# Kernel tuning notes

Measured on AMD Instinct MI355X. Metric: run time of the kernel, lower is better.

The kernel has to match this reference:

```python
import jax, jax.numpy as jnp
import numpy as np

B, C, N = 4, 64, 512
H = 128  # hidden width; MLP input is 2*C = 128


def setup_inputs() -> dict:
    key = jax.random.key(0)
    k0, k1, k2 = jax.random.split(key, 3)
    x = jax.random.normal(k0, (B, C, N), dtype=jnp.float32)
    # Torch Linear init ~ U(-1/sqrt(fan_in), 1/sqrt(fan_in)); stored as (in, out) for einsum.
    W1 = jax.random.normal(k1, (2 * C, H), dtype=jnp.float32) * (1.0 / np.sqrt(2 * C))
    b1 = jnp.zeros((H,), dtype=jnp.float32)
    W2 = jax.random.normal(k2, (H, 1), dtype=jnp.float32) * (1.0 / np.sqrt(H))
    b2 = jnp.zeros((1,), dtype=jnp.float32)
    return {"x": x, "W1": W1, "b1": b1, "W2": W2, "b2": b2}


def reference(x, W1, b1, W2, b2):
    # x: (B, C, N). Equivalent to the per-offset loop: for every pair (i, j) with
    # j > i, score = MLP(concat(x[:, :, i], x[:, :, j])), placed at y[:, i, j].
    # Dropout is identity in eval mode.
    b, c, n = x.shape
    xt = jnp.transpose(x, (0, 2, 1))                      # (B, N, C)
    left = jnp.broadcast_to(xt[:, :, None, :], (b, n, n, c))   # row index i
    right = jnp.broadcast_to(xt[:, None, :, :], (b, n, n, c))  # col index j
    pairs = jnp.concatenate([left, right], axis=-1)       # (B, N, N, 2C)
    h = jax.nn.relu(jnp.einsum('bijc,ch->bijh', pairs, W1) + b1)
    score = (jnp.einsum('bijh,ho->bijo', h, W2) + b2)[..., 0]  # (B, N, N)
    mask = jnp.triu(jnp.ones((n, n), dtype=score.dtype), k=1)  # strict upper triangle
    return score * mask
```

## Files before the change

### kernel.cpp

```cpp
#include <hip/hip_runtime.h>

#define B_ 4
#define C_ 64
#define N_ 512
#define H_ 128

typedef float v2f __attribute__((ext_vector_type(2)));
typedef float v4f __attribute__((ext_vector_type(4)));

__global__ __launch_bounds__(256) void proj_kernel(
    const float* __restrict__ x, const float* __restrict__ W1,
    const float* __restrict__ b1, float* __restrict__ Lbuf,
    float* __restrict__ Rbuf)
{
    __shared__ float Wl[64 * 128];
    __shared__ float xs[16 * 68];

    const int t    = threadIdx.x;
    const int half = blockIdx.x >> 7;
    const int rem  = blockIdx.x & 127;
    const int b    = rem >> 5;
    const int i0   = (rem & 31) * 16;
    const int cbase = half * 64;

    const float4* W14 = (const float4*)W1;
    float4* Wl4 = (float4*)Wl;
    #pragma unroll
    for (int k = 0; k < 8; ++k)
        Wl4[t + k * 256] = W14[cbase * 32 + t + k * 256];

    #pragma unroll
    for (int k = 0; k < 4; ++k) {
        int idx = t + k * 256;
        int c = idx >> 4, ii = idx & 15;
        xs[ii * 68 + c] = x[b * (C_ * N_) + c * N_ + i0 + ii];
    }
    __syncthreads();

    const int hq  = t & 31;
    const int il  = (t >> 5) * 2;
    const int col = hq * 4;

    v2f a0l = {0.f, 0.f}, a0h = {0.f, 0.f};
    if (half) {
        float4 bv = *(const float4*)(b1 + col);
        a0l = {bv.x, bv.y};
        a0h = {bv.z, bv.w};
    }
    v2f a1l = a0l, a1h = a0h;

    const v4f* Wlv = (const v4f*)Wl;
    #pragma unroll
    for (int c = 0; c < 64; c += 4) {
        float4 xv0 = *(float4*)(xs + il * 68 + c);
        float4 xv1 = *(float4*)(xs + (il + 1) * 68 + c);
        const float* x0p = (const float*)&xv0;
        const float* x1p = (const float*)&xv1;
        #pragma unroll
        for (int cc = 0; cc < 4; ++cc) {
            v4f wv = Wlv[(c + cc) * 32 + hq];
            v2f wl = wv.xy, wh = wv.zw;
            v2f xb0 = {x0p[cc], x0p[cc]};
            v2f xb1 = {x1p[cc], x1p[cc]};
            a0l = __builtin_elementwise_fma(wl, xb0, a0l);
            a0h = __builtin_elementwise_fma(wh, xb0, a0h);
            a1l = __builtin_elementwise_fma(wl, xb1, a1l);
            a1h = __builtin_elementwise_fma(wh, xb1, a1h);
        }
    }

    float* buf = half ? Rbuf : Lbuf;
    float* o = buf + b * (N_ * H_) + (i0 + il) * H_ + col;
    *(float4*)o        = make_float4(a0l.x, a0l.y, a0h.x, a0h.y);
    *(float4*)(o + H_) = make_float4(a1l.x, a1l.y, a1h.x, a1h.y);
}

__global__ __launch_bounds__(256) void pair_kernel(
    const float* __restrict__ Lbuf, const float* __restrict__ Rbuf,
    const float* __restrict__ W2, const float* __restrict__ b2,
    float* __restrict__ out)
{
    __shared__ v4f Lt4[32 * 32];
    __shared__ v4f Rt4[32 * 32];

    const int t = threadIdx.x;
    int b, it, jt;
    {
        int bid = blockIdx.x;
        if (bid >= 544) {
            int z = bid - 544;
            b = z & 3;
            int k = z >> 2;
            it = 1;
            while (k >= it) { k -= it; ++it; }
            jt = k;
            float* outb = out + b * (N_ * N_);
            const int r = t >> 3, cq = t & 7;
            *(float4*)(outb + (it * 32 + r) * N_ + jt * 32 + cq * 4) =
                make_float4(0.f, 0.f, 0.f, 0.f);
            return;
        }
        b = bid & 3;
        int k = bid >> 2;
        it = 0;
        while (k >= 16 - it) { k -= 16 - it; ++it; }
        jt = it + k;
    }
    const int ti0 = it * 32, tj0 = jt * 32;
    float* outb = out + b * (N_ * N_);

    const float* Lsrc = Lbuf + b * (N_ * H_) + ti0 * H_;
    const float* Rsrc = Rbuf + b * (N_ * H_) + tj0 * H_;
    #pragma unroll
    for (int kk = 0; kk < 4; ++kk) {
        int idx = t + kk * 256;
        int row = idx >> 5, hc = idx & 31;
        int sc = hc ^ (row >> 2);
        Lt4[row * 32 + sc] = *(const v4f*)(Lsrc + row * H_ + hc * 4);
        Rt4[row * 32 + sc] = *(const v4f*)(Rsrc + row * H_ + hc * 4);
    }
    __syncthreads();

    const int w    = t >> 6;
    const int lane = t & 63;
    const int til  = (w >> 1) * 16 + (lane >> 3) * 2;
    const int tjl  = (w & 1) * 16 + (lane & 7) * 2;
    const int rotL = til >> 2;
    const int rotR = tjl >> 2;

    const v4f* Lp  = Lt4 + til * 32;
    const v4f* Rp  = Rt4 + tjl * 32;
    const v4f* W24 = (const v4f*)W2;

    v2f c00l = {0.f, 0.f}, c00h = {0.f, 0.f};
    v2f c01l = {0.f, 0.f}, c01h = {0.f, 0.f};
    v2f c10l = {0.f, 0.f}, c10h = {0.f, 0.f};
    v2f c11l = {0.f, 0.f}, c11h = {0.f, 0.f};

    #pragma unroll 8
    for (int hc = 0; hc < 32; ++hc) {
        const int oL = hc ^ rotL;
        const int oR = hc ^ rotR;
        v4f L0 = Lp[oL];
        v4f L1 = Lp[32 + oL];
        v4f R0 = Rp[oR];
        v4f R1 = Rp[32 + oR];
        v4f wv = W24[hc];
        v2f wl = wv.xy, wh = wv.zw;
        const v2f z2 = {0.f, 0.f};
        v2f s;
        s = __builtin_elementwise_max(L0.xy + R0.xy, z2);
        c00l = __builtin_elementwise_fma(s, wl, c00l);
        s = __builtin_elementwise_max(L0.zw + R0.zw, z2);
        c00h = __builtin_elementwise_fma(s, wh, c00h);
        s = __builtin_elementwise_max(L0.xy + R1.xy, z2);
        c01l = __builtin_elementwise_fma(s, wl, c01l);
        s = __builtin_elementwise_max(L0.zw + R1.zw, z2);
        c01h = __builtin_elementwise_fma(s, wh, c01h);
        s = __builtin_elementwise_max(L1.xy + R0.xy, z2);
        c10l = __builtin_elementwise_fma(s, wl, c10l);
        s = __builtin_elementwise_max(L1.zw + R0.zw, z2);
        c10h = __builtin_elementwise_fma(s, wh, c10h);
        s = __builtin_elementwise_max(L1.xy + R1.xy, z2);
        c11l = __builtin_elementwise_fma(s, wl, c11l);
        s = __builtin_elementwise_max(L1.zw + R1.zw, z2);
        c11h = __builtin_elementwise_fma(s, wh, c11h);
    }

    const float bias2 = b2[0];
    float a00 = (c00l.x + c00l.y) + (c00h.x + c00h.y);
    float a01 = (c01l.x + c01l.y) + (c01h.x + c01h.y);
    float a10 = (c10l.x + c10l.y) + (c10h.x + c10h.y);
    float a11 = (c11l.x + c11l.y) + (c11h.x + c11h.y);

    const int gi0 = ti0 + til, gj0 = tj0 + tjl;
    float2 v0, v1;
    v0.x = (gj0     > gi0    ) ? (a00 + bias2) : 0.f;
    v0.y = (gj0 + 1 > gi0    ) ? (a01 + bias2) : 0.f;
    v1.x = (gj0     > gi0 + 1) ? (a10 + bias2) : 0.f;
    v1.y = (gj0 + 1 > gi0 + 1) ? (a11 + bias2) : 0.f;
    *(float2*)(outb + gi0 * N_ + gj0) = v0;
    *(float2*)(outb + (gi0 + 1) * N_ + gj0) = v1;
}

extern "C" void kernel_launch(void* const* d_in, const int* in_sizes, int n_in,
                              void* d_out, int out_size, void* d_ws, size_t ws_size,
                              hipStream_t stream)
{
    const float* x  = (const float*)d_in[0];
    const float* W1 = (const float*)d_in[1];
    const float* b1 = (const float*)d_in[2];
    const float* W2 = (const float*)d_in[3];
    const float* b2 = (const float*)d_in[4];
    float* out  = (float*)d_out;
    float* Lbuf = (float*)d_ws;
    float* Rbuf = Lbuf + B_ * N_ * H_;

    proj_kernel<<<256, 256, 0, stream>>>(x, W1, b1, Lbuf, Rbuf);
    pair_kernel<<<B_ * 256, 256, 0, stream>>>(Lbuf, Rbuf, W2, b2, out);
}
```

Before: 75.60 us.

## Fuse projection into pair kernel, recomputing L/R tiles per block

The separate projection kernel and its global L/R workspace are removed. Each pair-tile block now loads the 64 channels of x for its 32 row and 32 column positions into shared memory and computes the L and R projections itself, reading W1 from global or L2. The projections go straight into the swizzled shared tiles, which saves a kernel launch and the global write and read of the intermediate buffers. The cost is redundant projection work: each of the 544 active blocks recomputes 64 projected rows, and that work is comparable to or larger than its pairwise MLP work.

```diff
diff --git a/kernel.cpp b/kernel.cpp
--- a/kernel.cpp
+++ b/kernel.cpp
@@ -8,78 +8,14 @@
 typedef float v2f __attribute__((ext_vector_type(2)));
 typedef float v4f __attribute__((ext_vector_type(4)));
 
-__global__ __launch_bounds__(256) void proj_kernel(
+#define XS_STRIDE 72
+
+__global__ __launch_bounds__(256) void fused_kernel(
     const float* __restrict__ x, const float* __restrict__ W1,
-    const float* __restrict__ b1, float* __restrict__ Lbuf,
-    float* __restrict__ Rbuf)
+    const float* __restrict__ b1, const float* __restrict__ W2,
+    const float* __restrict__ b2, float* __restrict__ out)
 {
-    __shared__ float Wl[64 * 128];
-    __shared__ float xs[16 * 68];
-
-    const int t    = threadIdx.x;
-    const int half = blockIdx.x >> 7;
-    const int rem  = blockIdx.x & 127;
-    const int b    = rem >> 5;
-    const int i0   = (rem & 31) * 16;
-    const int cbase = half * 64;
-
-    const float4* W14 = (const float4*)W1;
-    float4* Wl4 = (float4*)Wl;
-    #pragma unroll
-    for (int k = 0; k < 8; ++k)
-        Wl4[t + k * 256] = W14[cbase * 32 + t + k * 256];
-
-    #pragma unroll
-    for (int k = 0; k < 4; ++k) {
-        int idx = t + k * 256;
-        int c = idx >> 4, ii = idx & 15;
-        xs[ii * 68 + c] = x[b * (C_ * N_) + c * N_ + i0 + ii];
-    }
-    __syncthreads();
-
-    const int hq  = t & 31;
-    const int il  = (t >> 5) * 2;
-    const int col = hq * 4;
-
-    v2f a0l = {0.f, 0.f}, a0h = {0.f, 0.f};
-    if (half) {
-        float4 bv = *(const float4*)(b1 + col);
-        a0l = {bv.x, bv.y};
-        a0h = {bv.z, bv.w};
-    }
-    v2f a1l = a0l, a1h = a0h;
-
-    const v4f* Wlv = (const v4f*)Wl;
-    #pragma unroll
-    for (int c = 0; c < 64; c += 4) {
-        float4 xv0 = *(float4*)(xs + il * 68 + c);
-        float4 xv1 = *(float4*)(xs + (il + 1) * 68 + c);
-        const float* x0p = (const float*)&xv0;
-        const float* x1p = (const float*)&xv1;
-        #pragma unroll
-        for (int cc = 0; cc < 4; ++cc) {
-            v4f wv = Wlv[(c + cc) * 32 + hq];
-            v2f wl = wv.xy, wh = wv.zw;
-            v2f xb0 = {x0p[cc], x0p[cc]};
-            v2f xb1 = {x1p[cc], x1p[cc]};
-            a0l = __builtin_elementwise_fma(wl, xb0, a0l);
-            a0h = __builtin_elementwise_fma(wh, xb0, a0h);
-            a1l = __builtin_elementwise_fma(wl, xb1, a1l);
-            a1h = __builtin_elementwise_fma(wh, xb1, a1h);
-        }
-    }
-
-    float* buf = half ? Rbuf : Lbuf;
-    float* o = buf + b * (N_ * H_) + (i0 + il) * H_ + col;
-    *(float4*)o        = make_float4(a0l.x, a0l.y, a0h.x, a0h.y);
-    *(float4*)(o + H_) = make_float4(a1l.x, a1l.y, a1h.x, a1h.y);
-}
-
-__global__ __launch_bounds__(256) void pair_kernel(
-    const float* __restrict__ Lbuf, const float* __restrict__ Rbuf,
-    const float* __restrict__ W2, const float* __restrict__ b2,
-    float* __restrict__ out)
-{
+    __shared__ float xs[64 * XS_STRIDE];
     __shared__ v4f Lt4[32 * 32];
     __shared__ v4f Rt4[32 * 32];
 
@@ -109,15 +45,63 @@
     const int ti0 = it * 32, tj0 = jt * 32;
     float* outb = out + b * (N_ * N_);
 
-    const float* Lsrc = Lbuf + b * (N_ * H_) + ti0 * H_;
-    const float* Rsrc = Rbuf + b * (N_ * H_) + tj0 * H_;
-    #pragma unroll
-    for (int kk = 0; kk < 4; ++kk) {
-        int idx = t + kk * 256;
-        int row = idx >> 5, hc = idx & 31;
-        int sc = hc ^ (row >> 2);
-        Lt4[row * 32 + sc] = *(const v4f*)(Lsrc + row * H_ + hc * 4);
-        Rt4[row * 32 + sc] = *(const v4f*)(Rsrc + row * H_ + hc * 4);
+    {
+        const float* xb = x + b * (C_ * N_);
+        #pragma unroll
+        for (int k = 0; k < 4; ++k) {
+            int idx = t + k * 256;
+            int c = idx >> 4, q = idx & 15;
+            int r0 = q * 4;
+            int gcol = (r0 < 32) ? (ti0 + r0) : (tj0 + (r0 - 32));
+            v4f v = *(const v4f*)(xb + c * N_ + gcol);
+            *(v4f*)(xs + c * XS_STRIDE + r0) = v;
+        }
+    }
+    __syncthreads();
+
+    {
+        const int hq = t & 31;
+        const int rg = t >> 5;
+        const int r0 = rg * 4;
+        const v4f* W14 = (const v4f*)W1;
+        v4f bv = *(const v4f*)(b1 + hq * 4);
+
+        v2f La[4][2], Ra[4][2];
+        #pragma unroll
+        for (int k = 0; k < 4; ++k) {
+            La[k][0] = (v2f){0.f, 0.f};
+            La[k][1] = (v2f){0.f, 0.f};
+            Ra[k][0] = (v2f){bv.x, bv.y};
+            Ra[k][1] = (v2f){bv.z, bv.w};
+        }
+
+        #pragma unroll 4
+        for (int c = 0; c < 64; ++c) {
+            v4f wl4 = W14[c * 32 + hq];
+            v4f wr4 = W14[(64 + c) * 32 + hq];
+            v4f xi = *(const v4f*)(xs + c * XS_STRIDE + r0);
+            v4f xj = *(const v4f*)(xs + c * XS_STRIDE + 32 + r0);
+            v2f wll = wl4.xy, wlh = wl4.zw;
+            v2f wrl = wr4.xy, wrh = wr4.zw;
+            #pragma unroll
+            for (int k = 0; k < 4; ++k) {
+                v2f xik = {xi[k], xi[k]};
+                v2f xjk = {xj[k], xj[k]};
+                La[k][0] = __builtin_elementwise_fma(wll, xik, La[k][0]);
+                La[k][1] = __builtin_elementwise_fma(wlh, xik, La[k][1]);
+                Ra[k][0] = __builtin_elementwise_fma(wrl, xjk, Ra[k][0]);
+                Ra[k][1] = __builtin_elementwise_fma(wrh, xjk, Ra[k][1]);
+            }
+        }
+
+        const int sc = hq ^ rg;
+        #pragma unroll
+        for (int k = 0; k < 4; ++k) {
+            Lt4[(r0 + k) * 32 + sc] =
+                (v4f){La[k][0].x, La[k][0].y, La[k][1].x, La[k][1].y};
+            Rt4[(r0 + k) * 32 + sc] =
+                (v4f){Ra[k][0].x, Ra[k][0].y, Ra[k][1].x, Ra[k][1].y};
+        }
     }
     __syncthreads();
 
@@ -192,10 +176,8 @@
     const float* b1 = (const float*)d_in[2];
     const float* W2 = (const float*)d_in[3];
     const float* b2 = (const float*)d_in[4];
-    float* out  = (float*)d_out;
-    float* Lbuf = (float*)d_ws;
-    float* Rbuf = Lbuf + B_ * N_ * H_;
+    float* out = (float*)d_out;
+    (void)d_ws; (void)ws_size;
 
-    proj_kernel<<<256, 256, 0, stream>>>(x, W1, b1, Lbuf, Rbuf);
-    pair_kernel<<<B_ * 256, 256, 0, stream>>>(Lbuf, Rbuf, W2, b2, out);
+    fused_kernel<<<1024, 256, 0, stream>>>(x, W1, b1, W2, b2, out);
 }
```

After: 80.81 us. +6.9%, slower.

## Widen pair tiles to 32x64 and move zero-fill into projection kernel

Applied to the files above, without the earlier changes.

Each pair block now covers a 32x64 output tile, so every thread computes 2x4 outputs. This doubles the reuse of the loaded L values and cuts the number of pair blocks. Zeroing of the lower-triangle tiles moves out of the pair kernel and into extra blocks of the projection kernel, so the pair grid holds only compute tiles. The trade-off is more accumulator registers and more LDS for the larger R tile, fewer blocks (288) to fill the CUs, and more wasted work on diagonal tiles.

```diff
diff --git a/kernel.cpp b/kernel.cpp
--- a/kernel.cpp
+++ b/kernel.cpp
@@ -8,15 +8,39 @@
 typedef float v2f __attribute__((ext_vector_type(2)));
 typedef float v4f __attribute__((ext_vector_type(4)));
 
-__global__ __launch_bounds__(256) void proj_kernel(
+__device__ __forceinline__ int zc_of(int it) {
+    return (it < 2) ? 0 : (((32 * it - 63) >> 6) + 1);
+}
+
+__global__ __launch_bounds__(256) void proj_zero_kernel(
     const float* __restrict__ x, const float* __restrict__ W1,
     const float* __restrict__ b1, float* __restrict__ Lbuf,
-    float* __restrict__ Rbuf)
+    float* __restrict__ Rbuf, float* __restrict__ out)
 {
     __shared__ float Wl[64 * 128];
     __shared__ float xs[16 * 68];
 
-    const int t    = threadIdx.x;
+    const int t = threadIdx.x;
+
+    if (blockIdx.x >= 256) {
+        int z = blockIdx.x - 256;
+        int b = z & 3;
+        int k = z >> 2;
+        int it = 0, jt2 = 0;
+        #pragma unroll 1
+        for (; it < 16; ++it) {
+            int c = zc_of(it);
+            if (k < c) { jt2 = k; break; }
+            k -= c;
+        }
+        float* outb = out + b * (N_ * N_);
+        const int r = t >> 3, q = t & 7;
+        float* p = outb + (it * 32 + r) * N_ + jt2 * 64 + q * 4;
+        *(float4*)p        = make_float4(0.f, 0.f, 0.f, 0.f);
+        *(float4*)(p + 32) = make_float4(0.f, 0.f, 0.f, 0.f);
+        return;
+    }
+
     const int half = blockIdx.x >> 7;
     const int rem  = blockIdx.x & 127;
     const int b    = rem >> 5;
@@ -44,8 +68,8 @@
     v2f a0l = {0.f, 0.f}, a0h = {0.f, 0.f};
     if (half) {
         float4 bv = *(const float4*)(b1 + col);
-        a0l = {bv.x, bv.y};
-        a0h = {bv.z, bv.w};
+        a0l = (v2f){bv.x, bv.y};
+        a0h = (v2f){bv.z, bv.w};
     }
     v2f a1l = a0l, a1h = a0h;
 
@@ -81,32 +105,19 @@
     float* __restrict__ out)
 {
     __shared__ v4f Lt4[32 * 32];
-    __shared__ v4f Rt4[32 * 32];
+    __shared__ v4f Rt4[64 * 32];
 
     const int t = threadIdx.x;
-    int b, it, jt;
-    {
-        int bid = blockIdx.x;
-        if (bid >= 544) {
-            int z = bid - 544;
-            b = z & 3;
-            int k = z >> 2;
-            it = 1;
-            while (k >= it) { k -= it; ++it; }
-            jt = k;
-            float* outb = out + b * (N_ * N_);
-            const int r = t >> 3, cq = t & 7;
-            *(float4*)(outb + (it * 32 + r) * N_ + jt * 32 + cq * 4) =
-                make_float4(0.f, 0.f, 0.f, 0.f);
-            return;
-        }
-        b = bid & 3;
-        int k = bid >> 2;
-        it = 0;
-        while (k >= 16 - it) { k -= 16 - it; ++it; }
-        jt = it + k;
-    }
-    const int ti0 = it * 32, tj0 = jt * 32;
+    const int b = blockIdx.x & 3;
+    int k = blockIdx.x >> 2;
+    int it = 0, jt2 = 0;
+    #pragma unroll 1
+    for (; it < 16; ++it) {
+        int wc = 8 - zc_of(it);
+        if (k < wc) { jt2 = zc_of(it) + k; break; }
+        k -= wc;
+    }
+    const int ti0 = it * 32, tj0 = jt2 * 64;
     float* outb = out + b * (N_ * N_);
 
     const float* Lsrc = Lbuf + b * (N_ * H_) + ti0 * H_;
@@ -117,6 +128,12 @@
         int row = idx >> 5, hc = idx & 31;
         int sc = hc ^ (row >> 2);
         Lt4[row * 32 + sc] = *(const v4f*)(Lsrc + row * H_ + hc * 4);
+    }
+    #pragma unroll
+    for (int kk = 0; kk < 8; ++kk) {
+        int idx = t + kk * 256;
+        int row = idx >> 5, hc = idx & 31;
+        int sc = hc ^ (row >> 2);
         Rt4[row * 32 + sc] = *(const v4f*)(Rsrc + row * H_ + hc * 4);
     }
     __syncthreads();
@@ -124,7 +141,7 @@
     const int w    = t >> 6;
     const int lane = t & 63;
     const int til  = (w >> 1) * 16 + (lane >> 3) * 2;
-    const int tjl  = (w & 1) * 16 + (lane & 7) * 2;
+    const int tjl  = (w & 1) * 32 + (lane & 7) * 4;
     const int rotL = til >> 2;
     const int rotR = tjl >> 2;
 
@@ -132,55 +149,59 @@
     const v4f* Rp  = Rt4 + tjl * 32;
     const v4f* W24 = (const v4f*)W2;
 
-    v2f c00l = {0.f, 0.f}, c00h = {0.f, 0.f};
-    v2f c01l = {0.f, 0.f}, c01h = {0.f, 0.f};
-    v2f c10l = {0.f, 0.f}, c10h = {0.f, 0.f};
-    v2f c11l = {0.f, 0.f}, c11h = {0.f, 0.f};
-
-    #pragma unroll 8
+    v2f acc[2][4][2];
+    #pragma unroll
+    for (int r = 0; r < 2; ++r)
+        #pragma unroll
+        for (int j = 0; j < 4; ++j) {
+            acc[r][j][0] = (v2f){0.f, 0.f};
+            acc[r][j][1] = (v2f){0.f, 0.f};
+        }
+
+    #pragma unroll 4
     for (int hc = 0; hc < 32; ++hc) {
         const int oL = hc ^ rotL;
         const int oR = hc ^ rotR;
-        v4f L0 = Lp[oL];
-        v4f L1 = Lp[32 + oL];
-        v4f R0 = Rp[oR];
-        v4f R1 = Rp[32 + oR];
+        v4f L[2], R[4];
+        L[0] = Lp[oL];
+        L[1] = Lp[32 + oL];
+        R[0] = Rp[oR];
+        R[1] = Rp[32 + oR];
+        R[2] = Rp[64 + oR];
+        R[3] = Rp[96 + oR];
         v4f wv = W24[hc];
         v2f wl = wv.xy, wh = wv.zw;
         const v2f z2 = {0.f, 0.f};
-        v2f s;
-        s = __builtin_elementwise_max(L0.xy + R0.xy, z2);
-        c00l = __builtin_elementwise_fma(s, wl, c00l);
-        s = __builtin_elementwise_max(L0.zw + R0.zw, z2);
-        c00h = __builtin_elementwise_fma(s, wh, c00h);
-        s = __builtin_elementwise_max(L0.xy + R1.xy, z2);
-        c01l = __builtin_elementwise_fma(s, wl, c01l);
-        s = __builtin_elementwise_max(L0.zw + R1.zw, z2);
-        c01h = __builtin_elementwise_fma(s, wh, c01h);
-        s = __builtin_elementwise_max(L1.xy + R0.xy, z2);
-        c10l = __builtin_elementwise_fma(s, wl, c10l);
-        s = __builtin_elementwise_max(L1.zw + R0.zw, z2);
-        c10h = __builtin_elementwise_fma(s, wh, c10h);
-        s = __builtin_elementwise_max(L1.xy + R1.xy, z2);
-        c11l = __builtin_elementwise_fma(s, wl, c11l);
-        s = __builtin_elementwise_max(L1.zw + R1.zw, z2);
-        c11h = __builtin_elementwise_fma(s, wh, c11h);
+        #pragma unroll
+        for (int r = 0; r < 2; ++r) {
+            v2f ll = L[r].xy, lh = L[r].zw;
+            #pragma unroll
+            for (int j = 0; j < 4; ++j) {
+                v2f s;
+                s = __builtin_elementwise_max(ll + R[j].xy, z2);
+                acc[r][j][0] = __builtin_elementwise_fma(s, wl, acc[r][j][0]);
+                s = __builtin_elementwise_max(lh + R[j].zw, z2);
+                acc[r][j][1] = __builtin_elementwise_fma(s, wh, acc[r][j][1]);
+            }
+        }
     }
 
     const float bias2 = b2[0];
-    float a00 = (c00l.x + c00l.y) + (c00h.x + c00h.y);
-    float a01 = (c01l.x + c01l.y) + (c01h.x + c01h.y);
-    float a10 = (c10l.x + c10l.y) + (c10h.x + c10h.y);
-    float a11 = (c11l.x + c11l.y) + (c11h.x + c11h.y);
-
     const int gi0 = ti0 + til, gj0 = tj0 + tjl;
-    float2 v0, v1;
-    v0.x = (gj0     > gi0    ) ? (a00 + bias2) : 0.f;
-    v0.y = (gj0 + 1 > gi0    ) ? (a01 + bias2) : 0.f;
-    v1.x = (gj0     > gi0 + 1) ? (a10 + bias2) : 0.f;
-    v1.y = (gj0 + 1 > gi0 + 1) ? (a11 + bias2) : 0.f;
-    *(float2*)(outb + gi0 * N_ + gj0) = v0;
-    *(float2*)(outb + (gi0 + 1) * N_ + gj0) = v1;
+    #pragma unroll
+    for (int r = 0; r < 2; ++r) {
+        float4 v;
+        float a0 = (acc[r][0][0].x + acc[r][0][0].y) + (acc[r][0][1].x + acc[r][0][1].y);
+        float a1 = (acc[r][1][0].x + acc[r][1][0].y) + (acc[r][1][1].x + acc[r][1][1].y);
+        float a2 = (acc[r][2][0].x + acc[r][2][0].y) + (acc[r][2][1].x + acc[r][2][1].y);
+        float a3 = (acc[r][3][0].x + acc[r][3][0].y) + (acc[r][3][1].x + acc[r][3][1].y);
+        const int gi = gi0 + r;
+        v.x = (gj0     > gi) ? (a0 + bias2) : 0.f;
+        v.y = (gj0 + 1 > gi) ? (a1 + bias2) : 0.f;
+        v.z = (gj0 + 2 > gi) ? (a2 + bias2) : 0.f;
+        v.w = (gj0 + 3 > gi) ? (a3 + bias2) : 0.f;
+        *(float4*)(outb + gi * N_ + gj0) = v;
+    }
 }
 
 extern "C" void kernel_launch(void* const* d_in, const int* in_sizes, int n_in,
@@ -196,6 +217,6 @@
     float* Lbuf = (float*)d_ws;
     float* Rbuf = Lbuf + B_ * N_ * H_;
 
-    proj_kernel<<<256, 256, 0, stream>>>(x, W1, b1, Lbuf, Rbuf);
-    pair_kernel<<<B_ * 256, 256, 0, stream>>>(Lbuf, Rbuf, W2, b2, out);
-}
+    proj_zero_kernel<<<480, 256, 0, stream>>>(x, W1, b1, Lbuf, Rbuf, out);
+    pair_kernel<<<288, 256, 0, stream>>>(Lbuf, Rbuf, W2, b2, out);
+}
```

Result: slower. 77.51 us (+2.5%).
